# Kernel tuning notes

Measured on AMD Instinct MI355X. Metric: run time of the kernel, lower is better.

The kernel has to match this reference:

```python
import jax, jax.numpy as jnp
import numpy as np

B, G, N, D = 4, 2, 2048, 512
H, DH = 8, 64
DI = H * DH  # dim_inner = 512


def setup_inputs() -> dict:
    key = jax.random.key(0)
    ks = jax.random.split(key, 5)
    x = jax.random.normal(ks[0], (B, G, N, D), jnp.float32)
    # grouped 1x1 convs == per-group linear layers
    Wq = jax.random.normal(ks[1], (G, DI, D), jnp.float32) / np.sqrt(D)
    Wkv = jax.random.normal(ks[2], (G, 2 * DI, D), jnp.float32) / np.sqrt(D)
    Wout = jax.random.normal(ks[3], (G, D, DI), jnp.float32) / np.sqrt(DI)
    null_kv = jax.random.normal(ks[4], (2, G, H, 1, DH), jnp.float32)
    # rotary angle tensors (ndim==2 path of the module)
    pos = jnp.arange(N, dtype=jnp.float32)
    inv_freq = 1.0 / (10000.0 ** (jnp.arange(0, DH, 2, dtype=jnp.float32) / DH))
    freqs = pos[:, None] * inv_freq[None, :]          # [N, DH/2]
    ang = jnp.concatenate([freqs, freqs], axis=-1)     # [N, DH]
    return {"x": x, "Wq": Wq, "Wkv": Wkv, "Wout": Wout,
            "null_kv": null_kv, "rot_q": ang, "rot_k": ang}


def _rotate_half(t):
    t1, t2 = jnp.split(t, 2, axis=-1)
    return jnp.concatenate([-t2, t1], axis=-1)


def _apply_rope(ang, t):
    # t: [b,g,h,n,dh], ang: [n,dh] broadcasts over b,g,h
    return t * jnp.cos(ang) + _rotate_half(t) * jnp.sin(ang)


def reference(x, Wq, Wkv, Wout, null_kv, rot_q, rot_k):
    b, g, n, d = x.shape
    h, dh = H, DH
    # grouped 1x1 conv projections (per-group linear)
    q = jnp.einsum('bgnd,ged->bgne', x, Wq)    # e = h*dh, h-major
    kv = jnp.einsum('bgnd,ged->bgne', x, Wkv)
    k, v = jnp.split(kv, 2, axis=-1)
    to_heads = lambda t: t.reshape(b, g, n, h, dh).transpose(0, 1, 3, 2, 4)  # b g h n dh
    q, k, v = map(to_heads, (q, k, v))
    # rotary position embedding
    q = _apply_rope(rot_q, q)
    k = _apply_rope(rot_k, k)
    # null key/value prepend
    nk = jnp.broadcast_to(null_kv[0][None], (b, g, h, 1, dh))
    nv = jnpp = None
    nv = jnp.broadcast_to(null_kv[1][None], (b, g, h, 1, dh))
    k = jnp.concatenate([nk, k], axis=-2)      # b g h (n+1) dh
    v = jnp.concatenate([nv, v], axis=-2)
    # scaled dot-product attention (non-causal, no mask)
    scale = dh ** -0.5
    attn = jax.nn.softmax(jnp.einsum('bghqd,bghkd->bghqk', q * scale, k), axis=-1)
    out = jnp.einsum('bghqk,bghkd->bghqd', attn, v)
    # merge heads: 'b g h n d -> b g n (h d)' then grouped 1x1 output conv
    out = out.transpose(0, 1, 3, 2, 4).reshape(b, g, n, h * dh)
    return jnp.einsum('bgne,gde->bgnd', out, Wout)
```

## Files before the change

kernel.cpp:

```cpp
#include <hip/hip_runtime.h>
#include <hip/hip_bf16.h>
#include <math.h>

#define Bn  4
#define Gn  2
#define Nn  2048
#define Dn  512
#define Hn  8
#define DHn 64
#define N1n 2049
#define NPAD 2112
#define BGH (Bn*Gn*Hn)

#define SCL 0.18033688011112042f

typedef short short8 __attribute__((ext_vector_type(8)));
typedef float float4v __attribute__((ext_vector_type(4)));

#define OB_B  ((size_t)0)
#define QB_B  ((size_t)16777216)
#define KB_B  ((size_t)33554432)
#define VT_B  ((size_t)50855936)
#define XB_B  ((size_t)68157440)
#define WC_B  ((size_t)84934656)
#define WO_B  ((size_t)88080384)
#define CSQ_B ((size_t)89128960)
#define CSK_B ((size_t)90177536)

static __device__ __forceinline__ unsigned short f2bf(float x) {
    union { float f; unsigned int u; } c; c.f = x;
    unsigned int r = c.u + 0x7fffu + ((c.u >> 16) & 1u);
    return (unsigned short)(r >> 16);
}

static __device__ __forceinline__ unsigned int pk2bf(float lo, float hi) {
    union { float f; unsigned int u; } a, b; a.f = lo; b.f = hi;
    return __builtin_amdgcn_perm(b.u + 0x8000u, a.u + 0x8000u, 0x07060302u);
}

static __device__ __forceinline__ void gload16(const void* g, void* l) {
    __builtin_amdgcn_global_load_lds(
        (const __attribute__((address_space(1))) void*)g,
        (__attribute__((address_space(3))) void*)l, 16, 0, 0);
}

#define S0 2097152
#define S1 393216
#define S2 131072
#define S3 32768
#define S4 32768
#define S5 8192
__global__ __launch_bounds__(256) void prep(const float* __restrict__ x,
                                            const float* __restrict__ Wq,
                                            const float* __restrict__ Wkv,
                                            const float* __restrict__ Wout,
                                            const float* __restrict__ nkv,
                                            const float* __restrict__ rot_q,
                                            const float* __restrict__ rot_k,
                                            char* __restrict__ wsb)
{
    const int idx = blockIdx.x * 256 + threadIdx.x;
    if (idx < S0) {
        float4 v = ((const float4*)x)[idx];
        ((ushort4*)(wsb + XB_B))[idx] =
            make_ushort4(f2bf(v.x), f2bf(v.y), f2bf(v.z), f2bf(v.w));
    } else if (idx < S0 + S1) {
        const int t = idx - S0;
        const int g = t / 196608;
        const int r4 = t - g * 196608;
        const int j = r4 * 4;
        const int row = j >> 9, k = j & 511;
        const float* src = (row < 512)
            ? (Wq  + ((size_t)g * 512  + row)        * 512 + k)
            : (Wkv + ((size_t)g * 1024 + (row - 512)) * 512 + k);
        float4 v = *(const float4*)src;
        ((ushort4*)(wsb + WC_B))[(size_t)g * 196608 + r4] =
            make_ushort4(f2bf(v.x), f2bf(v.y), f2bf(v.z), f2bf(v.w));
    } else if (idx < S0 + S1 + S2) {
        const int t = idx - (S0 + S1);
        float4 v = ((const float4*)Wout)[t];
        ((ushort4*)(wsb + WO_B))[t] =
            make_ushort4(f2bf(v.x), f2bf(v.y), f2bf(v.z), f2bf(v.w));
    } else if (idx < S0 + S1 + S2 + S3) {
        const int t = idx - (S0 + S1 + S2);
        float4 a = ((const float4*)rot_q)[t];
        float2* cs = (float2*)(wsb + CSQ_B);
        cs[t*4+0] = make_float2(cosf(a.x), sinf(a.x));
        cs[t*4+1] = make_float2(cosf(a.y), sinf(a.y));
        cs[t*4+2] = make_float2(cosf(a.z), sinf(a.z));
        cs[t*4+3] = make_float2(cosf(a.w), sinf(a.w));
    } else if (idx < S0 + S1 + S2 + S3 + S4) {
        const int t = idx - (S0 + S1 + S2 + S3);
        float4 a = ((const float4*)rot_k)[t];
        float2* cs = (float2*)(wsb + CSK_B);
        cs[t*4+0] = make_float2(cosf(a.x), sinf(a.x));
        cs[t*4+1] = make_float2(cosf(a.y), sinf(a.y));
        cs[t*4+2] = make_float2(cosf(a.z), sinf(a.z));
        cs[t*4+3] = make_float2(cosf(a.w), sinf(a.w));
    } else if (idx < S0 + S1 + S2 + S3 + S4 + S5) {
        const int t = idx - (S0 + S1 + S2 + S3 + S4);
        const int s = t >> 12, rem = t & 4095;
        const int bgh = rem >> 6, dh = rem & 63;
        const int gh = bgh & 15;
        if (s == 0)
            ((unsigned short*)(wsb + KB_B))[(size_t)bgh * NPAD * 64 + dh] =
                f2bf(nkv[gh * 64 + dh]);
        else
            ((unsigned short*)(wsb + VT_B))[((size_t)bgh * 64 + dh) * NPAD] =
                f2bf(nkv[1024 + gh * 64 + dh]);
    }
}
#define PREP_BLOCKS ((S0+S1+S2+S3+S4+S5)/256)

__global__ __launch_bounds__(256) void qkv_proj(char* __restrict__ wsb)
{
    __shared__ alignas(16) unsigned short As[128 * 64];
    __shared__ alignas(16) unsigned short Bs[128 * 64];

    const int g  = blockIdx.z;
    const int m0 = blockIdx.x * 128;
    const int e0 = blockIdx.y * 128;
    const int tid = threadIdx.x;
    const int wv = tid >> 6, ln = tid & 63;
    const int l15 = ln & 15, quad = ln >> 4;
    const int wm = (wv & 1) * 64, we = (wv >> 1) * 64;

    const unsigned short* xb = (const unsigned short*)(wsb + XB_B);
    const unsigned short* wc = (const unsigned short*)(wsb + WC_B);

    const int bq = m0 >> 11;
    const size_t arowbase = ((size_t)(bq * Gn + g) * Nn + (m0 & 2047));
    const size_t brockbase = ((size_t)g * 1536 + e0);

    float4v acc[4][4];
    #pragma unroll
    for (int i = 0; i < 4; ++i)
        #pragma unroll
        for (int j = 0; j < 4; ++j) acc[i][j] = (float4v){0.f,0.f,0.f,0.f};

    for (int k0 = 0; k0 < 512; k0 += 64) {
        #pragma unroll
        for (int it = 0; it < 4; ++it) {
            const int sb  = it * 256 + wv * 64;
            const int slot = sb + ln;
            const int row = slot >> 3;
            const int c8  = (slot & 7) ^ (row & 7);
            gload16(xb + (arowbase + row) * 512 + k0 + c8 * 8, &As[(size_t)sb * 8]);
            gload16(wc + (brockbase + row) * 512 + k0 + c8 * 8, &Bs[(size_t)sb * 8]);
        }
        __syncthreads();

        #pragma unroll
        for (int kh = 0; kh < 2; ++kh) {
            short8 af[4], bf[4];
            #pragma unroll
            for (int mi = 0; mi < 4; ++mi) {
                const int r = wm + mi * 16 + l15;
                af[mi] = *(const short8*)&As[r * 64 + (((kh*4+quad) ^ (r & 7)) << 3)];
            }
            #pragma unroll
            for (int ni = 0; ni < 4; ++ni) {
                const int r = we + ni * 16 + l15;
                bf[ni] = *(const short8*)&Bs[r * 64 + (((kh*4+quad) ^ (r & 7)) << 3)];
            }
            #pragma unroll
            for (int mi = 0; mi < 4; ++mi)
                #pragma unroll
                for (int ni = 0; ni < 4; ++ni)
                    acc[mi][ni] = __builtin_amdgcn_mfma_f32_16x16x32_bf16(
                        af[mi], bf[ni], acc[mi][ni], 0, 0, 0);
        }
        __syncthreads();
    }

    const int sec  = e0 >> 9;
    const int hoff = wv >> 1;
    const int nb   = (m0 & 2047) + wm;

    if (sec == 0) {
        unsigned short* Qb = (unsigned short*)(wsb + QB_B);
        const float2* cs = (const float2*)(wsb + CSQ_B);
        const int bgh = (bq * Gn + g) * Hn + ((e0 & 511) >> 6) + hoff;
        #pragma unroll
        for (int mi = 0; mi < 4; ++mi) {
            #pragma unroll
            for (int r = 0; r < 4; ++r) {
                const int n = nb + mi * 16 + quad * 4 + r;
                unsigned short* qrow = Qb + ((size_t)bgh * Nn + n) * 64;
                #pragma unroll
                for (int ni = 0; ni < 4; ++ni) {
                    const int dh = ni * 16 + l15;
                    float2 c = cs[n * 64 + dh];
                    const float v = acc[mi][ni][r];
                    const float p = acc[mi][ni ^ 2][r];
                    const float rh = (ni < 2) ? -p : p;
                    qrow[dh] = f2bf((v * c.x + rh * c.y) * SCL);
                }
            }
        }
    } else if (sec == 1) {
        unsigned short* Kb = (unsigned short*)(wsb + KB_B);
        const float2* cs = (const float2*)(wsb + CSK_B);
        const int bgh = (bq * Gn + g) * Hn + ((e0 - 512) >> 6) + hoff;
        #pragma unroll
        for (int mi = 0; mi < 4; ++mi) {
            #pragma unroll
            for (int r = 0; r < 4; ++r) {
                const int n = nb + mi * 16 + quad * 4 + r;
                unsigned short* krow = Kb + ((size_t)bgh * NPAD + n + 1) * 64;
                #pragma unroll
                for (int ni = 0; ni < 4; ++ni) {
                    const int dh = ni * 16 + l15;
                    float2 c = cs[n * 64 + dh];
                    const float v = acc[mi][ni][r];
                    const float p = acc[mi][ni ^ 2][r];
                    const float rh = (ni < 2) ? -p : p;
                    krow[dh] = f2bf(v * c.x + rh * c.y);
                }
            }
        }
    } else {
        unsigned short* Vt = (unsigned short*)(wsb + VT_B);
        const int bgh = (bq * Gn + g) * Hn + ((e0 - 1024) >> 6) + hoff;
        #pragma unroll
        for (int mi = 0; mi < 4; ++mi) {
            #pragma unroll
            for (int ni = 0; ni < 4; ++ni) {
                const int dh = ni * 16 + l15;
                unsigned short* vrow = Vt + ((size_t)bgh * 64 + dh) * NPAD
                                         + nb + mi * 16 + quad * 4 + 1;
                #pragma unroll
                for (int r = 0; r < 4; ++r)
                    vrow[r] = f2bf(acc[mi][ni][r]);
            }
        }
    }
}

__global__ __launch_bounds__(256, 4) void attn(const unsigned short* __restrict__ Qb,
                                               const unsigned short* __restrict__ Kb,
                                               const unsigned short* __restrict__ Vt,
                                               unsigned short* __restrict__ Ob)
{
    __shared__ alignas(16) unsigned short Ks[64 * 64];
    __shared__ alignas(16) unsigned short Vs[64 * 64];
    __shared__ alignas(16) unsigned short Ps[4 * 32 * 64];

    const int tid  = threadIdx.x;
    const int bid  = blockIdx.x;
    const int bgh  = bid >> 4;
    const int q0   = (bid & 15) * 128;
    const int wv   = tid >> 6;
    const int ln   = tid & 63;
    const int l15  = ln & 15;
    const int quad = ln >> 4;

    short8 bq[2][2];
    #pragma unroll
    for (int qs = 0; qs < 2; ++qs) {
        const unsigned short* qrow =
            Qb + ((size_t)bgh * Nn + q0 + wv * 32 + qs * 16 + l15) * 64;
        bq[qs][0] = *(const short8*)(qrow + quad * 8);
        bq[qs][1] = *(const short8*)(qrow + 32 + quad * 8);
    }

    float4v Oa[2][4];
    #pragma unroll
    for (int ms = 0; ms < 2; ++ms)
        #pragma unroll
        for (int nt = 0; nt < 4; ++nt) Oa[ms][nt] = (float4v){0.f,0.f,0.f,0.f};
    float lr[2] = {0.f, 0.f};

    const unsigned short* kptr = Kb + (size_t)bgh * NPAD * 64;
    const unsigned short* vptr = Vt + (size_t)bgh * 64 * NPAD;
    unsigned short* Pw = Ps + wv * 32 * 64;

    for (int kt = 0; kt <= 2048; kt += 64) {
        #pragma unroll
        for (int it = 0; it < 2; ++it) {
            const int sb  = it * 256 + wv * 64;
            const int slot = sb + ln;
            const int row = slot >> 3;
            const int c8  = (slot & 7) ^ (row & 7);
            gload16(kptr + (size_t)row * 64   + c8 * 8, &Ks[(size_t)sb * 8]);
            gload16(vptr + (size_t)row * NPAD + c8 * 8, &Vs[(size_t)sb * 8]);
        }
        __syncthreads();

        #pragma unroll
        for (int mt = 0; mt < 4; ++mt) {
            const int rk = mt * 16 + l15;
            short8 af0 = *(const short8*)&Ks[rk * 64 + (((    quad) ^ (rk & 7)) << 3)];
            short8 af1 = *(const short8*)&Ks[rk * 64 + (((4 + quad) ^ (rk & 7)) << 3)];
            #pragma unroll
            for (int qs = 0; qs < 2; ++qs) {
                float4v z = {0.f, 0.f, 0.f, 0.f};
                z = __builtin_amdgcn_mfma_f32_16x16x32_bf16(af0, bq[qs][0], z, 0, 0, 0);
                z = __builtin_amdgcn_mfma_f32_16x16x32_bf16(af1, bq[qs][1], z, 0, 0, 0);
                if (kt == 2048) {
                    #pragma unroll
                    for (int r = 0; r < 4; ++r)
                        if (mt * 16 + quad * 4 + r > 0) z[r] = -INFINITY;
                }
                float pv0 = __builtin_amdgcn_exp2f(z[0]);
                float pv1 = __builtin_amdgcn_exp2f(z[1]);
                float pv2 = __builtin_amdgcn_exp2f(z[2]);
                float pv3 = __builtin_amdgcn_exp2f(z[3]);
                lr[qs] += (pv0 + pv1) + (pv2 + pv3);
                uint2 w = make_uint2(pk2bf(pv0, pv1), pk2bf(pv2, pv3));
                const int rq = qs * 16 + l15;
                const int cq = mt * 2 + (quad >> 1);
                *(uint2*)&Pw[rq * 64 + ((cq ^ (rq & 7)) << 3) + (quad & 1) * 4] = w;
            }
        }

        short8 ap[2][2];
        #pragma unroll
        for (int ms = 0; ms < 2; ++ms) {
            const int rq = ms * 16 + l15;
            ap[ms][0] = *(const short8*)&Pw[rq * 64 + (((    quad) ^ (rq & 7)) << 3)];
            ap[ms][1] = *(const short8*)&Pw[rq * 64 + (((4 + quad) ^ (rq & 7)) << 3)];
        }
        #pragma unroll
        for (int nt = 0; nt < 4; ++nt) {
            const int rv = nt * 16 + l15;
            short8 b0 = *(const short8*)&Vs[rv * 64 + (((    quad) ^ (rv & 7)) << 3)];
            short8 b1 = *(const short8*)&Vs[rv * 64 + (((4 + quad) ^ (rv & 7)) << 3)];
            #pragma unroll
            for (int ms = 0; ms < 2; ++ms) {
                Oa[ms][nt] = __builtin_amdgcn_mfma_f32_16x16x32_bf16(ap[ms][0], b0, Oa[ms][nt], 0, 0, 0);
                Oa[ms][nt] = __builtin_amdgcn_mfma_f32_16x16x32_bf16(ap[ms][1], b1, Oa[ms][nt], 0, 0, 0);
            }
        }
        __syncthreads();

        kptr += 64 * 64;
        vptr += 64;
    }

    float inv[2];
    #pragma unroll
    for (int qs = 0; qs < 2; ++qs) {
        float l = lr[qs];
        l += __shfl_xor(l, 16);
        l += __shfl_xor(l, 32);
        inv[qs] = 1.f / l;
    }
    unsigned short* obase = Ob + ((size_t)bgh * Nn + q0 + wv * 32) * 64;
    #pragma unroll
    for (int ms = 0; ms < 2; ++ms) {
        #pragma unroll
        for (int r = 0; r < 4; ++r) {
            const float iv = __shfl(inv[ms], quad * 4 + r);
            #pragma unroll
            for (int nt = 0; nt < 4; ++nt)
                obase[(ms * 16 + quad * 4 + r) * 64 + nt * 16 + l15] =
                    f2bf(Oa[ms][nt][r] * iv);
        }
    }
}

__global__ __launch_bounds__(256) void out_proj(const char* __restrict__ wsb,
                                                float* __restrict__ out)
{
    __shared__ alignas(16) unsigned short As[128 * 64];
    __shared__ alignas(16) unsigned short Bs[128 * 64];

    const int g  = blockIdx.z;
    const int m0 = blockIdx.x * 128;
    const int c0 = blockIdx.y * 128;
    const int tid = threadIdx.x;
    const int wv = tid >> 6, ln = tid & 63;
    const int l15 = ln & 15, quad = ln >> 4;
    const int wm = (wv & 1) * 64, we = (wv >> 1) * 64;

    const unsigned short* Ob = (const unsigned short*)(wsb + OB_B);
    const unsigned short* Wo = (const unsigned short*)(wsb + WO_B);

    const int bq = m0 >> 11;
    const int n0 = m0 & 2047;

    float4v acc[4][4];
    #pragma unroll
    for (int i = 0; i < 4; ++i)
        #pragma unroll
        for (int j = 0; j < 4; ++j) acc[i][j] = (float4v){0.f,0.f,0.f,0.f};

    for (int k0 = 0; k0 < 512; k0 += 64) {
        const int h = k0 >> 6;
        const unsigned short* abase =
            Ob + (((size_t)(bq * Gn + g) * Hn + h) * Nn + n0) * 64;
        const unsigned short* bbase =
            Wo + ((size_t)g * 512 + c0) * 512 + k0;
        #pragma unroll
        for (int it = 0; it < 4; ++it) {
            const int sb  = it * 256 + wv * 64;
            const int slot = sb + ln;
            const int row = slot >> 3;
            const int c8  = (slot & 7) ^ (row & 7);
            gload16(abase + (size_t)row * 64  + c8 * 8, &As[(size_t)sb * 8]);
            gload16(bbase + (size_t)row * 512 + c8 * 8, &Bs[(size_t)sb * 8]);
        }
        __syncthreads();

        #pragma unroll
        for (int kh = 0; kh < 2; ++kh) {
            short8 af[4], bf[4];
            #pragma unroll
            for (int mi = 0; mi < 4; ++mi) {
                const int r = wm + mi * 16 + l15;
                af[mi] = *(const short8*)&As[r * 64 + (((kh*4+quad) ^ (r & 7)) << 3)];
            }
            #pragma unroll
            for (int ni = 0; ni < 4; ++ni) {
                const int r = we + ni * 16 + l15;
                bf[ni] = *(const short8*)&Bs[r * 64 + (((kh*4+quad) ^ (r & 7)) << 3)];
            }
            #pragma unroll
            for (int mi = 0; mi < 4; ++mi)
                #pragma unroll
                for (int ni = 0; ni < 4; ++ni)
                    acc[mi][ni] = __builtin_amdgcn_mfma_f32_16x16x32_bf16(
                        af[mi], bf[ni], acc[mi][ni], 0, 0, 0);
        }
        __syncthreads();
    }

    #pragma unroll
    for (int mi = 0; mi < 4; ++mi) {
        #pragma unroll
        for (int r = 0; r < 4; ++r) {
            const int n = n0 + wm + mi * 16 + quad * 4 + r;
            float* orow = out + ((size_t)(bq * Gn + g) * Nn + n) * Dn;
            #pragma unroll
            for (int ni = 0; ni < 4; ++ni)
                orow[c0 + we + ni * 16 + l15] = acc[mi][ni][r];
        }
    }
}

extern "C" void kernel_launch(void* const* d_in, const int* in_sizes, int n_in,
                              void* d_out, int out_size, void* d_ws, size_t ws_size,
                              hipStream_t stream)
{
    const float* x     = (const float*)d_in[0];
    const float* Wq    = (const float*)d_in[1];
    const float* Wkv   = (const float*)d_in[2];
    const float* Wout  = (const float*)d_in[3];
    const float* nkv   = (const float*)d_in[4];
    const float* rot_q = (const float*)d_in[5];
    const float* rot_k = (const float*)d_in[6];
    float* out = (float*)d_out;
    char* wsb  = (char*)d_ws;

    prep<<<dim3(PREP_BLOCKS), 256, 0, stream>>>(x, Wq, Wkv, Wout, nkv,
                                                rot_q, rot_k, wsb);

    qkv_proj<<<dim3(64, 12, 2), 256, 0, stream>>>(wsb);

    attn<<<dim3(BGH * 16), 256, 0, stream>>>((const unsigned short*)(wsb + QB_B),
                                             (const unsigned short*)(wsb + KB_B),
                                             (const unsigned short*)(wsb + VT_B),
                                             (unsigned short*)(wsb + OB_B));

    out_proj<<<dim3(64, 4, 2), 256, 0, stream>>>(wsb, out);
}
```

Baseline: 282.8 us.

## Split attention key tile across wave pairs with shared-memory output reduction

Reorganises the attention block so that each wave handles 64 query rows and one half of each 64-key tile, instead of 32 query rows and all keys. K fragments from shared memory are reused across four query sub-tiles, and the P tile shrinks to 32 columns per wave. Partial outputs and row sums from the two key halves are combined through shared memory at the end. This cuts K/V shared-memory reads per MFMA, at the cost of more accumulator registers and an extra reduction and sync in the epilogue.

Measured after the change: 467.6 us. +65.4%, slower.

```diff
diff --git a/kernel.cpp b/kernel.cpp
--- a/kernel.cpp
+++ b/kernel.cpp
@@ -242,9 +242,11 @@
                                                const unsigned short* __restrict__ Vt,
                                                unsigned short* __restrict__ Ob)
 {
-    __shared__ alignas(16) unsigned short Ks[64 * 64];
-    __shared__ alignas(16) unsigned short Vs[64 * 64];
-    __shared__ alignas(16) unsigned short Ps[4 * 32 * 64];
+    __shared__ alignas(16) char smem[33280];
+    unsigned short* Ks = (unsigned short*)smem;
+    unsigned short* Vs = (unsigned short*)(smem + 8192);
+    unsigned short* Ps = (unsigned short*)(smem + 16384);
+    float*          lrb = (float*)(smem + 32768);
 
     const int tid  = threadIdx.x;
     const int bid  = blockIdx.x;
@@ -254,26 +256,28 @@
     const int ln   = tid & 63;
     const int l15  = ln & 15;
     const int quad = ln >> 4;
-
-    short8 bq[2][2];
-    #pragma unroll
-    for (int qs = 0; qs < 2; ++qs) {
+    const int qh   = wv & 1;
+    const int kh2  = wv >> 1;
+
+    short8 bq[4][2];
+    #pragma unroll
+    for (int qs = 0; qs < 4; ++qs) {
         const unsigned short* qrow =
-            Qb + ((size_t)bgh * Nn + q0 + wv * 32 + qs * 16 + l15) * 64;
+            Qb + ((size_t)bgh * Nn + q0 + qh * 64 + qs * 16 + l15) * 64;
         bq[qs][0] = *(const short8*)(qrow + quad * 8);
         bq[qs][1] = *(const short8*)(qrow + 32 + quad * 8);
     }
 
-    float4v Oa[2][4];
-    #pragma unroll
-    for (int ms = 0; ms < 2; ++ms)
-        #pragma unroll
-        for (int nt = 0; nt < 4; ++nt) Oa[ms][nt] = (float4v){0.f,0.f,0.f,0.f};
-    float lr[2] = {0.f, 0.f};
+    float4v acc[4][4];
+    #pragma unroll
+    for (int qs = 0; qs < 4; ++qs)
+        #pragma unroll
+        for (int nt = 0; nt < 4; ++nt) acc[qs][nt] = (float4v){0.f,0.f,0.f,0.f};
+    float lr[4] = {0.f, 0.f, 0.f, 0.f};
 
     const unsigned short* kptr = Kb + (size_t)bgh * NPAD * 64;
     const unsigned short* vptr = Vt + (size_t)bgh * 64 * NPAD;
-    unsigned short* Pw = Ps + wv * 32 * 64;
+    unsigned short* Pw = Ps + wv * 64 * 32;
 
     for (int kt = 0; kt <= 2048; kt += 64) {
         #pragma unroll
@@ -288,19 +292,19 @@
         __syncthreads();
 
         #pragma unroll
-        for (int mt = 0; mt < 4; ++mt) {
-            const int rk = mt * 16 + l15;
+        for (int mt = 0; mt < 2; ++mt) {
+            const int rk = kh2 * 32 + mt * 16 + l15;
             short8 af0 = *(const short8*)&Ks[rk * 64 + (((    quad) ^ (rk & 7)) << 3)];
             short8 af1 = *(const short8*)&Ks[rk * 64 + (((4 + quad) ^ (rk & 7)) << 3)];
             #pragma unroll
-            for (int qs = 0; qs < 2; ++qs) {
+            for (int qs = 0; qs < 4; ++qs) {
                 float4v z = {0.f, 0.f, 0.f, 0.f};
                 z = __builtin_amdgcn_mfma_f32_16x16x32_bf16(af0, bq[qs][0], z, 0, 0, 0);
                 z = __builtin_amdgcn_mfma_f32_16x16x32_bf16(af1, bq[qs][1], z, 0, 0, 0);
                 if (kt == 2048) {
                     #pragma unroll
                     for (int r = 0; r < 4; ++r)
-                        if (mt * 16 + quad * 4 + r > 0) z[r] = -INFINITY;
+                        if (kh2 * 32 + mt * 16 + quad * 4 + r > 0) z[r] = -INFINITY;
                 }
                 float pv0 = __builtin_amdgcn_exp2f(z[0]);
                 float pv1 = __builtin_amdgcn_exp2f(z[1]);
@@ -310,27 +314,25 @@
                 uint2 w = make_uint2(pk2bf(pv0, pv1), pk2bf(pv2, pv3));
                 const int rq = qs * 16 + l15;
                 const int cq = mt * 2 + (quad >> 1);
-                *(uint2*)&Pw[rq * 64 + ((cq ^ (rq & 7)) << 3) + (quad & 1) * 4] = w;
-            }
-        }
-
-        short8 ap[2][2];
-        #pragma unroll
-        for (int ms = 0; ms < 2; ++ms) {
-            const int rq = ms * 16 + l15;
-            ap[ms][0] = *(const short8*)&Pw[rq * 64 + (((    quad) ^ (rq & 7)) << 3)];
-            ap[ms][1] = *(const short8*)&Pw[rq * 64 + (((4 + quad) ^ (rq & 7)) << 3)];
+                *(uint2*)&Pw[rq * 32 + ((cq ^ (rq & 3)) << 3) + (quad & 1) * 4] = w;
+            }
+        }
+
+        short8 ap[4];
+        #pragma unroll
+        for (int qs = 0; qs < 4; ++qs) {
+            const int rq = qs * 16 + l15;
+            ap[qs] = *(const short8*)&Pw[rq * 32 + ((quad ^ (rq & 3)) << 3)];
         }
         #pragma unroll
         for (int nt = 0; nt < 4; ++nt) {
             const int rv = nt * 16 + l15;
-            short8 b0 = *(const short8*)&Vs[rv * 64 + (((    quad) ^ (rv & 7)) << 3)];
-            short8 b1 = *(const short8*)&Vs[rv * 64 + (((4 + quad) ^ (rv & 7)) << 3)];
-            #pragma unroll
-            for (int ms = 0; ms < 2; ++ms) {
-                Oa[ms][nt] = __builtin_amdgcn_mfma_f32_16x16x32_bf16(ap[ms][0], b0, Oa[ms][nt], 0, 0, 0);
-                Oa[ms][nt] = __builtin_amdgcn_mfma_f32_16x16x32_bf16(ap[ms][1], b1, Oa[ms][nt], 0, 0, 0);
-            }
+            const int c  = kh2 * 4 + quad;
+            short8 bv = *(const short8*)&Vs[rv * 64 + ((c ^ (rv & 7)) << 3)];
+            #pragma unroll
+            for (int qs = 0; qs < 4; ++qs)
+                acc[qs][nt] = __builtin_amdgcn_mfma_f32_16x16x32_bf16(
+                    ap[qs], bv, acc[qs][nt], 0, 0, 0);
         }
         __syncthreads();
 
@@ -338,24 +340,50 @@
         vptr += 64;
     }
 
-    float inv[2];
-    #pragma unroll
-    for (int qs = 0; qs < 2; ++qs) {
+    float lsum[4];
+    #pragma unroll
+    for (int qs = 0; qs < 4; ++qs) {
         float l = lr[qs];
         l += __shfl_xor(l, 16);
         l += __shfl_xor(l, 32);
-        inv[qs] = 1.f / l;
-    }
-    unsigned short* obase = Ob + ((size_t)bgh * Nn + q0 + wv * 32) * 64;
-    #pragma unroll
-    for (int ms = 0; ms < 2; ++ms) {
-        #pragma unroll
-        for (int r = 0; r < 4; ++r) {
-            const float iv = __shfl(inv[ms], quad * 4 + r);
-            #pragma unroll
-            for (int nt = 0; nt < 4; ++nt)
-                obase[(ms * 16 + quad * 4 + r) * 64 + nt * 16 + l15] =
-                    f2bf(Oa[ms][nt][r] * iv);
+        lsum[qs] = l;
+    }
+
+    float* Of = (float*)smem;
+    if (kh2 == 1) {
+        #pragma unroll
+        for (int qs = 0; qs < 4; ++qs)
+            #pragma unroll
+            for (int r = 0; r < 4; ++r) {
+                float* orow = Of + (qh * 64 + qs * 16 + quad * 4 + r) * 64;
+                #pragma unroll
+                for (int nt = 0; nt < 4; ++nt)
+                    orow[nt * 16 + l15] = acc[qs][nt][r];
+            }
+        if (quad == 0) {
+            #pragma unroll
+            for (int qs = 0; qs < 4; ++qs)
+                lrb[qh * 64 + qs * 16 + l15] = lsum[qs];
+        }
+    }
+    __syncthreads();
+    if (kh2 == 0) {
+        float inv[4];
+        #pragma unroll
+        for (int qs = 0; qs < 4; ++qs)
+            inv[qs] = 1.f / (lsum[qs] + lrb[qh * 64 + qs * 16 + l15]);
+        unsigned short* obase = Ob + ((size_t)bgh * Nn + q0 + qh * 64) * 64;
+        #pragma unroll
+        for (int qs = 0; qs < 4; ++qs) {
+            #pragma unroll
+            for (int r = 0; r < 4; ++r) {
+                const float iv = __shfl(inv[qs], quad * 4 + r);
+                const float* orow = Of + (qh * 64 + qs * 16 + quad * 4 + r) * 64;
+                #pragma unroll
+                for (int nt = 0; nt < 4; ++nt)
+                    obase[(qs * 16 + quad * 4 + r) * 64 + nt * 16 + l15] =
+                        f2bf((acc[qs][nt][r] + orow[nt * 16 + l15]) * iv);
+            }
         }
     }
 }
```
